# Optimization experiments

Hardware: AMD Instinct MI355X
Metric: run time of the kernel (lower is better)

Reference implementation:

```python
import jax, jax.numpy as jnp
import numpy as np

T_IN, B, H = 12, 65536, 64
T_OUT = 12
OVERLAP = 3


def setup_inputs() -> dict:
    key = jax.random.key(0)
    ks = jax.random.split(key, 9)
    return {
        "encoder_out": jax.random.normal(ks[0], (T_IN, B, H), dtype=jnp.float32),
        "encoder_hid": jax.random.normal(ks[1], (B, H), dtype=jnp.float32),
        "last": jax.random.normal(ks[2], (B, OVERLAP), dtype=jnp.float32),
        # GRUCell params (PyTorch layout: weight_ih (3H, in), weight_hh (3H, H), gate order r,z,n)
        "W_ih": jax.random.normal(ks[3], (3 * H, OVERLAP), dtype=jnp.float32) * 0.1,
        "W_hh": jax.random.normal(ks[4], (3 * H, H), dtype=jnp.float32) * 0.1,
        "b_ih": jax.random.normal(ks[5], (3 * H,), dtype=jnp.float32) * 0.1,
        "b_hh": jax.random.normal(ks[6], (3 * H,), dtype=jnp.float32) * 0.1,
        # Linear hidden -> 1
        "W_lin": jax.random.normal(ks[7], (1, H), dtype=jnp.float32) * 0.1,
        "b_lin": jax.random.normal(ks[8], (1,), dtype=jnp.float32) * 0.1,
    }


def _gru_cell(x, h, W_ih, W_hh, b_ih, b_hh):
    gi = x @ W_ih.T + b_ih  # (B, 3H)
    gh = h @ W_hh.T + b_hh  # (B, 3H)
    i_r, i_z, i_n = jnp.split(gi, 3, axis=-1)
    h_r, h_z, h_n = jnp.split(gh, 3, axis=-1)
    r = jax.nn.sigmoid(i_r + h_r)
    z = jax.nn.sigmoid(i_z + h_z)
    n = jnp.tanh(i_n + r * h_n)
    return (1.0 - z) * n + z * h


def reference(encoder_out, encoder_hid, last, W_ih, W_hh, b_ih, b_hh, W_lin, b_lin):
    def step(carry, _):
        hidden, lst = carry
        # attention over encoder time steps (softmax along time axis 0)
        attn_w = jnp.einsum('tbk,bk->tb', encoder_out, hidden)
        attn_w = jax.nn.softmax(attn_w, axis=0)
        context = jnp.einsum('tbk,tb->bk', encoder_out, attn_w)
        hidden = hidden + context
        hidden = _gru_cell(lst, hidden, W_ih, W_hh, b_ih, b_hh)
        out = hidden @ W_lin.T + b_lin  # (B, 1)
        # torch uses out.detach() when feeding back
        lst = jnp.concatenate([jax.lax.stop_gradient(out), lst[:, :OVERLAP - 1]], axis=-1)
        return (hidden, lst), out

    (_, _), outs = jax.lax.scan(step, (encoder_hid, last), None, length=T_OUT)
    # outs: (T_OUT, B, 1) -> (B, T_OUT), matching torch.cat(decoder_out, dim=-1)
    return jnp.transpose(outs[:, :, 0], (1, 0))
```

## Files before the change

kernel.cpp:

```cpp
#include <hip/hip_runtime.h>


#define TT 12
#define BB 65536
#define HH 64

typedef _Float16 half8 __attribute__((ext_vector_type(8)));
typedef _Float16 half4 __attribute__((ext_vector_type(4)));
typedef float    f32x4 __attribute__((ext_vector_type(4)));

__device__ __forceinline__ float sigm(float x){ return 1.0f/(1.0f+__expf(-x)); }
__device__ __forceinline__ float tanh_(float x){ return 1.0f - 2.0f/(__expf(2.0f*x)+1.0f); }

template<int N>
__device__ __forceinline__ float ror_add(float x){
    int s = __builtin_amdgcn_update_dpp(0, __float_as_int(x), 0x120+N, 0xF, 0xF, false);
    return x + __int_as_float(s);
}
__device__ __forceinline__ float sum16(float x){
    x = ror_add<1>(x); x = ror_add<2>(x); x = ror_add<4>(x); x = ror_add<8>(x);
    return x;
}

__global__ __launch_bounds__(256)
void decoder_kernel(const float* __restrict__ enc,
                    const float* __restrict__ hid0,
                    const float* __restrict__ last0,
                    const float* __restrict__ Wih,
                    const float* __restrict__ Whh,
                    const float* __restrict__ bih,
                    const float* __restrict__ bhh,
                    const float* __restrict__ Wlin,
                    const float* __restrict__ blin,
                    float* __restrict__ out)
{
    __shared__ __align__(16) _Float16 sHi[16*72];
    __shared__ __align__(16) _Float16 sLo[16*72];
    __shared__ __align__(16) float    sGh[16*196];

    const int tid  = threadIdx.x;
    const int wv   = tid >> 6;
    const int lane = tid & 63;
    const int q    = lane & 15;
    const int quad = lane >> 4;
    const int m    = wv*4 + quad;
    const size_t b = (size_t)blockIdx.x*16 + m;

    f32x4 e4[TT];
    #pragma unroll
    for (int t=0;t<TT;++t)
        e4[t] = *(const f32x4*)(enc + ((size_t)t*BB + b)*HH + 4*q);

    f32x4 h = *(const f32x4*)(hid0 + b*HH + 4*q);
    float l0 = last0[b*3+0], l1 = last0[b*3+1], l2 = last0[b*3+2];

    float wih[3][3][4];
    #pragma unroll
    for (int g=0; g<3; ++g)
        #pragma unroll
        for (int j=0;j<4;++j){
            int row = g*64 + 4*q + j;
            wih[g][0][j] = Wih[row*3+0];
            wih[g][1][j] = Wih[row*3+1];
            wih[g][2][j] = Wih[row*3+2];
        }
    float bc0[4], bc1[4], bi2[4], bh2[4];
    #pragma unroll
    for (int j=0;j<4;++j){
        bc0[j] = bih[0*64+4*q+j] + bhh[0*64+4*q+j];
        bc1[j] = bih[1*64+4*q+j] + bhh[1*64+4*q+j];
        bi2[j] = bih[2*64+4*q+j];
        bh2[j] = bhh[2*64+4*q+j];
    }
    f32x4 wl = *(const f32x4*)(Wlin + 4*q);
    float bl = blin[0];

    half8 wfhi[3][2], wflo[3][2];
    #pragma unroll
    for (int c=0;c<3;++c){
        int jout = (wv*3+c)*16 + q;
        #pragma unroll
        for (int kc=0;kc<2;++kc){
            const float* src = Whh + jout*64 + kc*32 + quad*8;
            half8 vh, vl;
            #pragma unroll
            for (int jj=0;jj<8;++jj){
                float w = src[jj];
                _Float16 whi = (_Float16)w;
                vh[jj] = whi;
                vl[jj] = (_Float16)(w - (float)whi);
            }
            wfhi[c][kc] = vh;
            wflo[c][kc] = vl;
        }
    }

    for (int s=0;s<TT;++s){
        float a[TT];
        #pragma unroll
        for (int t=0;t<TT;++t){
            float p = e4[t][0]*h[0] + e4[t][1]*h[1] + e4[t][2]*h[2] + e4[t][3]*h[3];
            a[t] = sum16(p);
        }
        float mx = a[0];
        #pragma unroll
        for (int t=1;t<TT;++t) mx = fmaxf(mx,a[t]);
        float ss = 0.f;
        #pragma unroll
        for (int t=0;t<TT;++t){ a[t] = __expf(a[t]-mx); ss += a[t]; }
        float inv = 1.0f/ss;
        #pragma unroll
        for (int t=0;t<TT;++t){
            float w = a[t]*inv;
            #pragma unroll
            for (int j=0;j<4;++j) h[j] += w * e4[t][j];
        }

        half4 hhi, hlo;
        #pragma unroll
        for (int j=0;j<4;++j){
            _Float16 hh = (_Float16)h[j];
            hhi[j] = hh;
            hlo[j] = (_Float16)(h[j] - (float)hh);
        }
        *(half4*)&sHi[m*72 + 4*q] = hhi;
        *(half4*)&sLo[m*72 + 4*q] = hlo;
        __syncthreads();

        half8 ahi0 = *(half8*)&sHi[q*72 +  0 + quad*8];
        half8 ahi1 = *(half8*)&sHi[q*72 + 32 + quad*8];
        half8 alo0 = *(half8*)&sLo[q*72 +  0 + quad*8];
        half8 alo1 = *(half8*)&sLo[q*72 + 32 + quad*8];
        #pragma unroll
        for (int c=0;c<3;++c){
            f32x4 acc = {0.f,0.f,0.f,0.f};
            acc = __builtin_amdgcn_mfma_f32_16x16x32_f16(ahi0, wfhi[c][0], acc, 0,0,0);
            acc = __builtin_amdgcn_mfma_f32_16x16x32_f16(ahi1, wfhi[c][1], acc, 0,0,0);
            acc = __builtin_amdgcn_mfma_f32_16x16x32_f16(ahi0, wflo[c][0], acc, 0,0,0);
            acc = __builtin_amdgcn_mfma_f32_16x16x32_f16(ahi1, wflo[c][1], acc, 0,0,0);
            acc = __builtin_amdgcn_mfma_f32_16x16x32_f16(alo0, wfhi[c][0], acc, 0,0,0);
            acc = __builtin_amdgcn_mfma_f32_16x16x32_f16(alo1, wfhi[c][1], acc, 0,0,0);
            int jcol = (wv*3+c)*16 + q;
            #pragma unroll
            for (int r=0;r<4;++r)
                sGh[(quad*4+r)*196 + jcol] = acc[r];
        }
        __syncthreads();

        f32x4 ghr = *(f32x4*)&sGh[m*196 +   0 + 4*q];
        f32x4 ghz = *(f32x4*)&sGh[m*196 +  64 + 4*q];
        f32x4 ghn = *(f32x4*)&sGh[m*196 + 128 + 4*q];

        float o = 0.f;
        #pragma unroll
        for (int j=0;j<4;++j){
            float gr = bc0[j] + wih[0][0][j]*l0 + wih[0][1][j]*l1 + wih[0][2][j]*l2 + ghr[j];
            float gz = bc1[j] + wih[1][0][j]*l0 + wih[1][1][j]*l1 + wih[1][2][j]*l2 + ghz[j];
            float gn = bi2[j] + wih[2][0][j]*l0 + wih[2][1][j]*l1 + wih[2][2][j]*l2;
            float r = sigm(gr);
            float z = sigm(gz);
            float n = tanh_(gn + r*(ghn[j] + bh2[j]));
            float hn = (1.f - z)*n + z*h[j];
            h[j] = hn;
            o += hn * wl[j];
        }
        o = sum16(o) + bl;
        if (q == 0) out[b*TT + s] = o;
        l2 = l1; l1 = l0; l0 = o;
    }
}

extern "C" void kernel_launch(void* const* d_in, const int* in_sizes, int n_in,
                              void* d_out, int out_size, void* d_ws, size_t ws_size,
                              hipStream_t stream)
{
    const float* enc  = (const float*)d_in[0];
    const float* hid0 = (const float*)d_in[1];
    const float* lst  = (const float*)d_in[2];
    const float* Wih  = (const float*)d_in[3];
    const float* Whh  = (const float*)d_in[4];
    const float* bih  = (const float*)d_in[5];
    const float* bhh  = (const float*)d_in[6];
    const float* Wlin = (const float*)d_in[7];
    const float* blin = (const float*)d_in[8];
    decoder_kernel<<<BB/16, 256, 0, stream>>>(enc, hid0, lst, Wih, Whh, bih, bhh,
                                              Wlin, blin, (float*)d_out);
}
```

Measured before the change: 452.8 us.

## Move GRU input weights and biases to shared memory to raise occupancy

Per-lane GRU input weights, biases and linear weights now live in a shared-memory table that is reloaded each step, instead of being held in registers for the whole kernel. Launch bounds now request 3 blocks per CU. The softmax normalisation is also deferred so the context is accumulated unnormalised and scaled once. The aim is to free VGPRs for higher occupancy. The cost is extra LDS reads every step and one more barrier.

```diff
diff --git a/kernel.cpp b/kernel.cpp
--- a/kernel.cpp
+++ b/kernel.cpp
@@ -22,7 +22,9 @@
     return x;
 }
 
-__global__ __launch_bounds__(256)
+#define CSTR 60
+
+__global__ __launch_bounds__(256, 3)
 void decoder_kernel(const float* __restrict__ enc,
                     const float* __restrict__ hid0,
                     const float* __restrict__ last0,
@@ -37,6 +39,7 @@
     __shared__ __align__(16) _Float16 sHi[16*72];
     __shared__ __align__(16) _Float16 sLo[16*72];
     __shared__ __align__(16) float    sGh[16*196];
+    __shared__ __align__(16) float    sConst[16*CSTR];
 
     const int tid  = threadIdx.x;
     const int wv   = tid >> 6;
@@ -46,6 +49,24 @@
     const int m    = wv*4 + quad;
     const size_t b = (size_t)blockIdx.x*16 + m;
 
+    for (int n = tid; n < 16*56; n += 256){
+        int qq = n / 56, s = n % 56;
+        float v;
+        if (s < 36){
+            int g = s/12, i = (s%12)/4, j = s%4;
+            v = Wih[(g*64 + 4*qq + j)*3 + i];
+        } else if (s < 52){
+            int t2 = s - 36, which = t2/4, j = t2%4;
+            if      (which == 0) v = bih[      4*qq+j] + bhh[      4*qq+j];
+            else if (which == 1) v = bih[ 64 + 4*qq+j] + bhh[ 64 + 4*qq+j];
+            else if (which == 2) v = bih[128 + 4*qq+j];
+            else                 v = bhh[128 + 4*qq+j];
+        } else {
+            v = Wlin[4*qq + (s-52)];
+        }
+        sConst[qq*CSTR + s] = v;
+    }
+
     f32x4 e4[TT];
     #pragma unroll
     for (int t=0;t<TT;++t)
@@ -53,26 +74,6 @@
 
     f32x4 h = *(const f32x4*)(hid0 + b*HH + 4*q);
     float l0 = last0[b*3+0], l1 = last0[b*3+1], l2 = last0[b*3+2];
-
-    float wih[3][3][4];
-    #pragma unroll
-    for (int g=0; g<3; ++g)
-        #pragma unroll
-        for (int j=0;j<4;++j){
-            int row = g*64 + 4*q + j;
-            wih[g][0][j] = Wih[row*3+0];
-            wih[g][1][j] = Wih[row*3+1];
-            wih[g][2][j] = Wih[row*3+2];
-        }
-    float bc0[4], bc1[4], bi2[4], bh2[4];
-    #pragma unroll
-    for (int j=0;j<4;++j){
-        bc0[j] = bih[0*64+4*q+j] + bhh[0*64+4*q+j];
-        bc1[j] = bih[1*64+4*q+j] + bhh[1*64+4*q+j];
-        bi2[j] = bih[2*64+4*q+j];
-        bh2[j] = bhh[2*64+4*q+j];
-    }
-    f32x4 wl = *(const f32x4*)(Wlin + 4*q);
     float bl = blin[0];
 
     half8 wfhi[3][2], wflo[3][2];
@@ -95,6 +96,10 @@
         }
     }
 
+    __syncthreads();
+
+    const float* cq = &sConst[q*CSTR];
+
     for (int s=0;s<TT;++s){
         float a[TT];
         #pragma unroll
@@ -109,12 +114,14 @@
         #pragma unroll
         for (int t=0;t<TT;++t){ a[t] = __expf(a[t]-mx); ss += a[t]; }
         float inv = 1.0f/ss;
+        f32x4 ctx = {0.f,0.f,0.f,0.f};
         #pragma unroll
         for (int t=0;t<TT;++t){
-            float w = a[t]*inv;
             #pragma unroll
-            for (int j=0;j<4;++j) h[j] += w * e4[t][j];
-        }
+            for (int j=0;j<4;++j) ctx[j] += a[t] * e4[t][j];
+        }
+        #pragma unroll
+        for (int j=0;j<4;++j) h[j] += ctx[j]*inv;
 
         half4 hhi, hlo;
         #pragma unroll
@@ -151,12 +158,19 @@
         f32x4 ghz = *(f32x4*)&sGh[m*196 +  64 + 4*q];
         f32x4 ghn = *(f32x4*)&sGh[m*196 + 128 + 4*q];
 
+        f32x4 wr0 = *(const f32x4*)(cq+ 0), wr1 = *(const f32x4*)(cq+ 4), wr2 = *(const f32x4*)(cq+ 8);
+        f32x4 wz0 = *(const f32x4*)(cq+12), wz1 = *(const f32x4*)(cq+16), wz2 = *(const f32x4*)(cq+20);
+        f32x4 wn0 = *(const f32x4*)(cq+24), wn1 = *(const f32x4*)(cq+28), wn2 = *(const f32x4*)(cq+32);
+        f32x4 bc0 = *(const f32x4*)(cq+36), bc1 = *(const f32x4*)(cq+40);
+        f32x4 bi2 = *(const f32x4*)(cq+44), bh2 = *(const f32x4*)(cq+48);
+        f32x4 wl  = *(const f32x4*)(cq+52);
+
         float o = 0.f;
         #pragma unroll
         for (int j=0;j<4;++j){
-            float gr = bc0[j] + wih[0][0][j]*l0 + wih[0][1][j]*l1 + wih[0][2][j]*l2 + ghr[j];
-            float gz = bc1[j] + wih[1][0][j]*l0 + wih[1][1][j]*l1 + wih[1][2][j]*l2 + ghz[j];
-            float gn = bi2[j] + wih[2][0][j]*l0 + wih[2][1][j]*l1 + wih[2][2][j]*l2;
+            float gr = bc0[j] + wr0[j]*l0 + wr1[j]*l1 + wr2[j]*l2 + ghr[j];
+            float gz = bc1[j] + wz0[j]*l0 + wz1[j]*l1 + wz2[j]*l2 + ghz[j];
+            float gn = bi2[j] + wn0[j]*l0 + wn1[j]*l1 + wn2[j]*l2;
             float r = sigm(gr);
             float z = sigm(gz);
             float n = tanh_(gn + r*(ghn[j] + bh2[j]));
```

Result: no change. 444.2 us (-1.9%).
